# Optimization experiments

Measured on AMD Instinct MI355X. Metric: run time of the kernel, lower is better.

## Reference

```python
import jax, jax.numpy as jnp
import numpy as np

B = 4096      # batch of states
N = 32        # SVGD particles per state
D_ACT = 16    # action dim
D_OBS = 64    # obs dim
H = 256       # critic hidden width
STEPS = 3     # num_svgd_steps
LR = 0.1      # svgd_lr
LIMIT = 1.0   # act_limit


def q_mlp(obs, x, w1, b1, w2, b2, w3, b3):
    # SAC-style critic: q(obs, a) -> scalar per row. obs/x: [BN, *]
    h = jnp.concatenate([obs, x], axis=-1)
    h = jax.nn.relu(h @ w1 + b1)
    h = jax.nn.relu(h @ w2 + b2)
    return (h @ w3 + b3)[..., 0]  # [BN]


def rbf_kernel(X, Y):
    # X: [B, N, D] (differentiable), Y: [B, N, D] (detached copy of X)
    diff = X[:, :, None, :] - Y[:, None, :, :]          # [B, N, N, D]
    dist_sq = jnp.sum(diff * diff, axis=-1)             # [B, N, N]
    # median heuristic bandwidth per batch element
    med = jnp.median(dist_sq.reshape(dist_sq.shape[0], -1), axis=-1)
    h = med / np.log(N) + 1e-8
    gamma = jax.lax.stop_gradient(1.0 / (2.0 * h))      # [B]
    K = jnp.exp(-gamma[:, None, None] * dist_sq)        # [B, N, N]
    # dK/dX (grad wrt first argument)
    K_grad = -2.0 * gamma[:, None, None, None] * diff * K[..., None]  # [B,N,N,D]
    return K, diff, gamma, K_grad


def setup_inputs() -> dict:
    key = jax.random.key(0)
    ks = jax.random.split(key, 6)
    BN = B * N
    sc = lambda k, shp: jax.random.normal(k, shp, jnp.float32) * 0.05
    return {
        "obs": jax.random.normal(ks[0], (BN, D_OBS), jnp.float32),
        "a": jax.random.normal(ks[1], (BN, D_ACT), jnp.float32),
        "w1": sc(ks[2], (D_OBS + D_ACT, H)),
        "b1": jnp.zeros((H,), jnp.float32),
        "w2": sc(ks[3], (H, H)),
        "b2": jnp.zeros((H,), jnp.float32),
        "w3": sc(ks[4], (H, 1)),
        "b3": jnp.zeros((1,), jnp.float32),
    }


def reference(obs, a, w1, b1, w2, b2, w3, b3):
    # a0 arrives detached in the original (sampler(obs, a0.detach(), ...))
    a = jax.lax.stop_gradient(a)
    logp = jnp.zeros((B, N), jnp.float32)
    q_fn = lambda X: q_mlp(obs, X, w1, b1, w2, b2, w3, b3)
    q_vals = None
    for _ in range(STEPS):
        # log_prob = min(q1, q1) == q1; score = d(sum q)/dX via vjp
        q_vals, vjp_fn = jax.vjp(q_fn, a)                 # q_vals: [BN]
        score, = vjp_fn(jnp.ones_like(q_vals))            # [BN, D_ACT]
        X = a.reshape(B, N, D_ACT)
        S = score.reshape(B, N, D_ACT)
        K, diff, gamma, K_grad = rbf_kernel(X, jax.lax.stop_gradient(X))
        # phi = (K.detach() @ score - K_grad.sum(2)) / N
        drive = jnp.einsum('bij,bjd->bid', jax.lax.stop_gradient(K), S)
        phi = (drive - K_grad.sum(axis=2)) / N            # [B, N, D]
        # logp correction terms
        tmp1 = (K_grad * S[:, None, :, :]).sum(-1).mean(-1)                 # [B, N]
        tmp2 = -2.0 * gamma[:, None] * (((-K_grad) * diff).sum(-1)
                                        - D_ACT * K).mean(-1)               # [B, N]
        logp = logp - LR * (tmp1 + tmp2)
        # svgd_optim + clamp + detach
        a = a + LR * phi.reshape(B * N, D_ACT)
        a = jax.lax.stop_gradient(jnp.clip(a, -LIMIT, LIMIT))
    return a.reshape(B, N, D_ACT), logp, q_vals
```

## Files before the change

### kernel.cpp

```cpp
#include <hip/hip_runtime.h>
#include <hip/hip_bf16.h>
#include <math.h>

#define BNROWS (4096*32)
#define RB     64
#define LN32   3.4657359027997265f

typedef __attribute__((ext_vector_type(8))) short bf16x8;
typedef __attribute__((ext_vector_type(4))) float f32x4;

static __device__ __forceinline__ ushort f2bf(float x) {
    union { __hip_bfloat16 h; ushort u; } cv;
    cv.h = __float2bfloat16(x);
    return cv.u;
}

__global__ void prep_all(const float* __restrict__ obs,
                         ushort* __restrict__ obs_bf,
                         const float* __restrict__ w1,
                         const float* __restrict__ w2,
                         ushort* __restrict__ pB1, ushort* __restrict__ pB2,
                         ushort* __restrict__ pB3, ushort* __restrict__ pB4) {
    if (blockIdx.x < 8192) {
        size_t i = ((size_t)blockIdx.x * 256 + threadIdx.x) * 4;
        float4 v = *(const float4*)&obs[i];
        ushort4 o;
        o.x = f2bf(v.x); o.y = f2bf(v.y); o.z = f2bf(v.z); o.w = f2bf(v.w);
        *(ushort4*)&obs_bf[i] = o;
        return;
    }
    int g = (blockIdx.x - 8192) * 256 + threadIdx.x;
    ushort out[8];
    ushort* dst;
    if (g < 3072) {
        int lane = g & 63, gc = g >> 6;
        int t = gc / 3, c = gc % 3;
        int m = lane & 15, q = lane >> 4, n = t * 16 + m;
        #pragma unroll
        for (int j = 0; j < 8; ++j) {
            int k = c * 32 + q * 8 + j;
            out[j] = f2bf((k < 80) ? w1[k * 256 + n] : 0.f);
        }
        dst = &pB1[g * 8];
    } else if (g < 11264) {
        int gg = g - 3072;
        int lane = gg & 63, gc = gg >> 6;
        int t = gc >> 3, c = gc & 7;
        int m = lane & 15, q = lane >> 4, n = t * 16 + m;
        #pragma unroll
        for (int j = 0; j < 8; ++j)
            out[j] = f2bf(w2[(c * 32 + q * 8 + j) * 256 + n]);
        dst = &pB2[gg * 8];
    } else if (g < 19456) {
        int gg = g - 11264;
        int lane = gg & 63, gc = gg >> 6;
        int t = gc >> 3, c = gc & 7;
        int m = lane & 15, q = lane >> 4;
        #pragma unroll
        for (int j = 0; j < 8; ++j)
            out[j] = f2bf(w2[(t * 16 + m) * 256 + c * 32 + q * 8 + j]);
        dst = &pB3[gg * 8];
    } else if (g < 19968) {
        int gg = g - 19456;
        int lane = gg & 63, c = gg >> 6;
        int m = lane & 15, q = lane >> 4;
        #pragma unroll
        for (int j = 0; j < 8; ++j)
            out[j] = f2bf(w1[(64 + m) * 256 + c * 32 + q * 8 + j]);
        dst = &pB4[gg * 8];
    } else return;
    *(uint4*)dst = *(uint4*)out;
}

__global__ __launch_bounds__(512) void mlp_mfma(
    const ushort* __restrict__ obs_bf,
    const float* __restrict__ a_in,
    const float* __restrict__ b1,
    const float* __restrict__ b2,
    const float* __restrict__ w3,
    const float* __restrict__ b3,
    const ushort* __restrict__ pB1, const ushort* __restrict__ pB2,
    const ushort* __restrict__ pB3, const ushort* __restrict__ pB4,
    float* __restrict__ score,
    float* __restrict__ qout)
{
    __shared__ __align__(16) ushort B0[RB * 264];
    __shared__ __align__(16) ushort B1s[RB * 104];
    __shared__ float qpart[8][RB];
    __shared__ float bias1[256], bias2[256], w3s[256];

    const int tid  = threadIdx.x;
    const int row0 = blockIdx.x * RB;

    {
        int r = tid >> 3, ch = tid & 7;
        *(uint4*)&B1s[r * 104 + ch * 8] =
            *(const uint4*)&obs_bf[(size_t)(row0 + r) * 64 + ch * 8];
    }
    if (tid < 256) {
        int r = tid >> 2, d0 = (tid & 3) * 4;
        float4 av = *(const float4*)&a_in[(size_t)(row0 + r) * 16 + d0];
        ushort4 pv;
        pv.x = f2bf(av.x); pv.y = f2bf(av.y); pv.z = f2bf(av.z); pv.w = f2bf(av.w);
        *(ushort4*)&B1s[r * 104 + 64 + d0] = pv;
        ushort4 zv; zv.x = zv.y = zv.z = zv.w = 0;
        *(ushort4*)&B1s[r * 104 + 80 + d0] = zv;
        bias1[tid] = b1[tid]; bias2[tid] = b2[tid]; w3s[tid] = w3[tid];
    }
    __syncthreads();

    const int lane = tid & 63;
    const int w    = tid >> 6;
    const int m    = lane & 15;
    const int q    = lane >> 4;
    const int qk   = q * 8;

    f32x4 acc[4][2];
    unsigned relumask = 0u;

    #pragma unroll
    for (int tc = 0; tc < 2; ++tc)
        #pragma unroll
        for (int rt = 0; rt < 4; ++rt) acc[rt][tc] = (f32x4){0.f, 0.f, 0.f, 0.f};
    for (int c = 0; c < 3; ++c) {
        bf16x8 af[4];
        #pragma unroll
        for (int rt = 0; rt < 4; ++rt)
            af[rt] = *(const bf16x8*)&B1s[(rt * 16 + m) * 104 + c * 32 + qk];
        #pragma unroll
        for (int tc = 0; tc < 2; ++tc) {
            bf16x8 wfr = *(const bf16x8*)&pB1[(((w * 2 + tc) * 3 + c) * 64 + lane) * 8];
            #pragma unroll
            for (int rt = 0; rt < 4; ++rt)
                acc[rt][tc] = __builtin_amdgcn_mfma_f32_16x16x32_bf16(wfr, af[rt], acc[rt][tc], 0, 0, 0);
        }
    }
    #pragma unroll
    for (int tc = 0; tc < 2; ++tc) {
        const float4 bv = *(const float4*)&bias1[(w * 2 + tc) * 16 + q * 4];
        const float bva[4] = {bv.x, bv.y, bv.z, bv.w};
        #pragma unroll
        for (int rt = 0; rt < 4; ++rt) {
            ushort4 pk;
            float z0 = acc[rt][tc][0] + bva[0];
            float z1 = acc[rt][tc][1] + bva[1];
            float z2 = acc[rt][tc][2] + bva[2];
            float z3 = acc[rt][tc][3] + bva[3];
            if (z0 > 0.f) relumask |= 1u << (rt * 8 + tc * 4 + 0);
            if (z1 > 0.f) relumask |= 1u << (rt * 8 + tc * 4 + 1);
            if (z2 > 0.f) relumask |= 1u << (rt * 8 + tc * 4 + 2);
            if (z3 > 0.f) relumask |= 1u << (rt * 8 + tc * 4 + 3);
            pk.x = f2bf(fmaxf(z0, 0.f)); pk.y = f2bf(fmaxf(z1, 0.f));
            pk.z = f2bf(fmaxf(z2, 0.f)); pk.w = f2bf(fmaxf(z3, 0.f));
            *(ushort4*)&B0[(rt * 16 + m) * 264 + (w * 2 + tc) * 16 + q * 4] = pk;
        }
    }
    __syncthreads();

    #pragma unroll
    for (int tc = 0; tc < 2; ++tc)
        #pragma unroll
        for (int rt = 0; rt < 4; ++rt) acc[rt][tc] = (f32x4){0.f, 0.f, 0.f, 0.f};
    for (int c = 0; c < 8; ++c) {
        bf16x8 af[4];
        #pragma unroll
        for (int rt = 0; rt < 4; ++rt)
            af[rt] = *(const bf16x8*)&B0[(rt * 16 + m) * 264 + c * 32 + qk];
        #pragma unroll
        for (int tc = 0; tc < 2; ++tc) {
            bf16x8 wfr = *(const bf16x8*)&pB2[(((w * 2 + tc) * 8 + c) * 64 + lane) * 8];
            #pragma unroll
            for (int rt = 0; rt < 4; ++rt)
                acc[rt][tc] = __builtin_amdgcn_mfma_f32_16x16x32_bf16(wfr, af[rt], acc[rt][tc], 0, 0, 0);
        }
    }
    __syncthreads();
    {
        float qp[4] = {0.f, 0.f, 0.f, 0.f};
        #pragma unroll
        for (int tc = 0; tc < 2; ++tc) {
            const float4 bv = *(const float4*)&bias2[(w * 2 + tc) * 16 + q * 4];
            const float4 wv = *(const float4*)&w3s[(w * 2 + tc) * 16 + q * 4];
            const float bva[4] = {bv.x, bv.y, bv.z, bv.w};
            const float wva[4] = {wv.x, wv.y, wv.z, wv.w};
            #pragma unroll
            for (int rt = 0; rt < 4; ++rt) {
                ushort4 pk; float dz[4];
                #pragma unroll
                for (int i = 0; i < 4; ++i) {
                    float z = acc[rt][tc][i] + bva[i];
                    if (z > 0.f) { qp[rt] += z * wva[i]; dz[i] = wva[i]; }
                    else         { dz[i] = 0.f; }
                }
                pk.x = f2bf(dz[0]); pk.y = f2bf(dz[1]);
                pk.z = f2bf(dz[2]); pk.w = f2bf(dz[3]);
                *(ushort4*)&B0[(rt * 16 + m) * 264 + (w * 2 + tc) * 16 + q * 4] = pk;
            }
        }
        #pragma unroll
        for (int rt = 0; rt < 4; ++rt) {
            float v = qp[rt];
            v += __shfl_xor(v, 16); v += __shfl_xor(v, 32);
            if (q == 0) qpart[w][rt * 16 + m] = v;
        }
    }
    __syncthreads();

    if (tid < RB) {
        float qs = b3[0];
        #pragma unroll
        for (int ww = 0; ww < 8; ++ww) qs += qpart[ww][tid];
        qout[row0 + tid] = qs;
    }

    #pragma unroll
    for (int tc = 0; tc < 2; ++tc)
        #pragma unroll
        for (int rt = 0; rt < 4; ++rt) acc[rt][tc] = (f32x4){0.f, 0.f, 0.f, 0.f};
    for (int c = 0; c < 8; ++c) {
        bf16x8 af[4];
        #pragma unroll
        for (int rt = 0; rt < 4; ++rt)
            af[rt] = *(const bf16x8*)&B0[(rt * 16 + m) * 264 + c * 32 + qk];
        #pragma unroll
        for (int tc = 0; tc < 2; ++tc) {
            bf16x8 wfr = *(const bf16x8*)&pB3[(((w * 2 + tc) * 8 + c) * 64 + lane) * 8];
            #pragma unroll
            for (int rt = 0; rt < 4; ++rt)
                acc[rt][tc] = __builtin_amdgcn_mfma_f32_16x16x32_bf16(wfr, af[rt], acc[rt][tc], 0, 0, 0);
        }
    }
    __syncthreads();
    #pragma unroll
    for (int rt = 0; rt < 4; ++rt)
        #pragma unroll
        for (int tc = 0; tc < 2; ++tc) {
            ushort4 pk;
            pk.x = f2bf((relumask >> (rt * 8 + tc * 4 + 0)) & 1u ? acc[rt][tc][0] : 0.f);
            pk.y = f2bf((relumask >> (rt * 8 + tc * 4 + 1)) & 1u ? acc[rt][tc][1] : 0.f);
            pk.z = f2bf((relumask >> (rt * 8 + tc * 4 + 2)) & 1u ? acc[rt][tc][2] : 0.f);
            pk.w = f2bf((relumask >> (rt * 8 + tc * 4 + 3)) & 1u ? acc[rt][tc][3] : 0.f);
            *(ushort4*)&B0[(rt * 16 + m) * 264 + (w * 2 + tc) * 16 + q * 4] = pk;
        }
    __syncthreads();

    if (w < 4) {
        f32x4 acc2 = (f32x4){0.f, 0.f, 0.f, 0.f};
        for (int c = 0; c < 8; ++c) {
            bf16x8 af = *(const bf16x8*)&B0[(w * 16 + m) * 264 + c * 32 + qk];
            bf16x8 wfr = *(const bf16x8*)&pB4[(c * 64 + lane) * 8];
            acc2 = __builtin_amdgcn_mfma_f32_16x16x32_bf16(wfr, af, acc2, 0, 0, 0);
        }
        float4 o; o.x = acc2[0]; o.y = acc2[1]; o.z = acc2[2]; o.w = acc2[3];
        *(float4*)&score[(size_t)(row0 + w * 16 + m) * 16 + q * 4] = o;
    }
}

__global__ __launch_bounds__(256, 2) void svgd4(
    const float* __restrict__ a_in,
    const float* __restrict__ score,
    const float* __restrict__ logp_in,
    float* __restrict__ logp_out,
    float* __restrict__ a_out,
    int first)
{
    __shared__ __align__(16) float X4[4][32 * 20];
    __shared__ __align__(16) float S4[4][32 * 20];
    __shared__ __align__(16) float KM4[4][1024];

    const int tid    = threadIdx.x;
    const int wv     = tid >> 6;
    const int lane   = tid & 63;
    const int stateg = blockIdx.x * 4 + wv;
    const size_t base = (size_t)stateg * 512;

    float* X  = X4[wv];
    float* S  = S4[wv];
    float* KM = KM4[wv];
    int*   h  = (int*)KM4[wv];

    {
        int g0 = lane * 8;
        int r = g0 >> 4, d0 = g0 & 15;
        float4 va0 = *(const float4*)&a_in[base + g0];
        float4 va1 = *(const float4*)&a_in[base + g0 + 4];
        float4 vs0 = *(const float4*)&score[base + g0];
        float4 vs1 = *(const float4*)&score[base + g0 + 4];
        *(float4*)&X[r * 20 + d0]     = va0;
        *(float4*)&X[r * 20 + d0 + 4] = va1;
        *(float4*)&S[r * 20 + d0]     = vs0;
        *(float4*)&S[r * 20 + d0 + 4] = vs1;
    }
    __asm__ volatile("s_waitcnt lgkmcnt(0)" ::: "memory");

    const int half = lane >> 5;
    const int j    = lane & 31;

    float Xj[16], Sj[16];
    #pragma unroll
    for (int d0 = 0; d0 < 16; d0 += 4) {
        float4 xv = *(const float4*)&X[j * 20 + d0];
        float4 sv = *(const float4*)&S[j * 20 + d0];
        Xj[d0 + 0] = xv.x; Xj[d0 + 1] = xv.y; Xj[d0 + 2] = xv.z; Xj[d0 + 3] = xv.w;
        Sj[d0 + 0] = sv.x; Sj[d0 + 1] = sv.y; Sj[d0 + 2] = sv.z; Sj[d0 + 3] = sv.w;
    }

    unsigned v[16]; float p[16];
    #pragma unroll 4
    for (int t = 0; t < 16; ++t) {
        const float* Xi = &X[(half * 16 + t) * 20];
        float ss = 0.f, pp = 0.f;
        #pragma unroll
        for (int d0 = 0; d0 < 16; d0 += 4) {
            float4 xv = *(const float4*)&Xi[d0];
            float df0 = xv.x - Xj[d0 + 0];
            float df1 = xv.y - Xj[d0 + 1];
            float df2 = xv.z - Xj[d0 + 2];
            float df3 = xv.w - Xj[d0 + 3];
            ss = fmaf(df0, df0, ss); pp = fmaf(df0, Sj[d0 + 0], pp);
            ss = fmaf(df1, df1, ss); pp = fmaf(df1, Sj[d0 + 1], pp);
            ss = fmaf(df2, df2, ss); pp = fmaf(df2, Sj[d0 + 2], pp);
            ss = fmaf(df3, df3, ss); pp = fmaf(df3, Sj[d0 + 3], pp);
        }
        v[t] = __float_as_uint(ss);
        p[t] = pp;
    }

    unsigned prefix = 0;
    int rank = 511;
    #pragma unroll 1
    for (int pass = 0; pass < 4; ++pass) {
        const int sh = 24 - pass * 8;
        int4 z4; z4.x = z4.y = z4.z = z4.w = 0;
        *(int4*)&h[lane * 4] = z4;
        __asm__ volatile("s_waitcnt lgkmcnt(0)" ::: "memory");
        #pragma unroll
        for (int t = 0; t < 16; ++t) {
            bool ok = (pass == 0) || ((v[t] >> (sh + 8)) == prefix);
            if (ok) atomicAdd(&h[(v[t] >> sh) & 255], 1);
        }
        __asm__ volatile("s_waitcnt lgkmcnt(0)" ::: "memory");
        int4 c4 = *(const int4*)&h[lane * 4];
        int c[4] = {c4.x, c4.y, c4.z, c4.w};
        int ct = c[0] + c[1] + c[2] + c[3];
        int inc = ct;
        #pragma unroll
        for (int off = 1; off < 64; off <<= 1) {
            int tt = __shfl_up(inc, off, 64);
            if (lane >= off) inc += tt;
        }
        int run = inc - ct;
        int binf = -1, runf = 0;
        #pragma unroll
        for (int e = 0; e < 4; ++e) {
            if (binf < 0 && rank >= run && rank < run + c[e]) {
                binf = lane * 4 + e; runf = run;
            }
            run += c[e];
        }
        unsigned long long bm = __ballot(binf >= 0);
        int src = __ffsll(bm) - 1;
        int bin  = __shfl(binf, src);
        int excl = __shfl(runf, src);
        prefix = (prefix << 8) | (unsigned)bin;
        rank -= excl;
    }
    const float v1 = __uint_as_float(prefix);

    int cle = 0;
    unsigned mgt = 0xFFFFFFFFu;
    #pragma unroll
    for (int t = 0; t < 16; ++t) {
        if (v[t] <= prefix) cle++;
        else mgt = min(mgt, v[t]);
    }
    #pragma unroll
    for (int off = 1; off < 64; off <<= 1) {
        cle += __shfl_xor(cle, off);
        mgt = min(mgt, (unsigned)__shfl_xor((int)mgt, off));
    }
    const float v2  = (cle >= 513) ? v1 : __uint_as_float(mgt);
    const float med = 0.5f * (v1 + v2);
    const float gamma = 1.0f / (2.0f * (med / LN32 + 1e-8f));

    #pragma unroll 4
    for (int t = 0; t < 16; ++t) {
        int i = half * 16 + t;
        float kk = __expf(-gamma * __uint_as_float(v[t]));
        KM[i * 32 + (j ^ i)] = kk;
        float acc = fmaf(fmaf(2.f * gamma, __uint_as_float(v[t]), -16.f), kk,
                         kk * p[t]);
        #pragma unroll
        for (int off = 1; off < 32; off <<= 1)
            acc += __shfl_xor(acc, off);
        if (j == 0) {
            float tmp = -2.f * gamma * acc * (1.f / 32.f);
            float prev = first ? 0.f : logp_in[stateg * 32 + i];
            logp_out[stateg * 32 + i] = prev - 0.1f * tmp;
        }
    }
    __asm__ volatile("s_waitcnt lgkmcnt(0)" ::: "memory");

    {
        const int d  = lane & 15;
        const int i0 = lane >> 4;
        float s1[8], s2[8], xi[8];
        #pragma unroll
        for (int e = 0; e < 8; ++e) {
            s1[e] = 0.f; s2[e] = 0.f;
            xi[e] = X[(i0 + 4 * e) * 20 + d];
        }
        for (int jj = 0; jj < 32; ++jj) {
            float xjv = X[jj * 20 + d];
            float sjv = S[jj * 20 + d];
            #pragma unroll
            for (int e = 0; e < 8; ++e) {
                int i = i0 + 4 * e;
                float kk = KM[i * 32 + (jj ^ i)];
                s1[e] = fmaf(kk, sjv, s1[e]);
                s2[e] = fmaf(kk, xi[e] - xjv, s2[e]);
            }
        }
        #pragma unroll
        for (int e = 0; e < 8; ++e) {
            int i = i0 + 4 * e;
            float phi = (s1[e] + 2.f * gamma * s2[e]) * (1.f / 32.f);
            float av = xi[e] + 0.1f * phi;
            av = fminf(fmaxf(av, -1.f), 1.f);
            a_out[base + i * 16 + d] = av;
        }
    }
}

extern "C" void kernel_launch(void* const* d_in, const int* in_sizes, int n_in,
                              void* d_out, int out_size, void* d_ws, size_t ws_size,
                              hipStream_t stream) {
    const float* obs = (const float*)d_in[0];
    const float* a0  = (const float*)d_in[1];
    const float* w1  = (const float*)d_in[2];
    const float* b1  = (const float*)d_in[3];
    const float* w2  = (const float*)d_in[4];
    const float* b2  = (const float*)d_in[5];
    const float* w3  = (const float*)d_in[6];
    const float* b3  = (const float*)d_in[7];

    float* out_a    = (float*)d_out;
    float* out_logp = out_a + (size_t)BNROWS * 16;
    float* out_q    = out_logp + BNROWS;

    char* p = (char*)d_ws;
    ushort* pB1 = (ushort*)p; p += 24576 * 2;
    ushort* pB2 = (ushort*)p; p += 65536 * 2;
    ushort* pB3 = (ushort*)p; p += 65536 * 2;
    ushort* pB4 = (ushort*)p; p += 4096 * 2;
    ushort* obs_bf = (ushort*)p; p += (size_t)BNROWS * 64 * 2;
    float* abuf0 = (float*)p; p += (size_t)BNROWS * 16 * 4;
    float* abuf1 = (float*)p; p += (size_t)BNROWS * 16 * 4;
    float* scr   = (float*)p; p += (size_t)BNROWS * 16 * 4;
    float* logp  = (float*)p; p += (size_t)BNROWS * 4;
    float* qtmp  = (float*)p;

    prep_all<<<8270, 256, 0, stream>>>(obs, obs_bf, w1, w2, pB1, pB2, pB3, pB4);

    const int MB = BNROWS / RB;
    const int SB = 4096 / 4;

    mlp_mfma<<<MB, 512, 0, stream>>>(obs_bf, a0, b1, b2, w3, b3,
                                     pB1, pB2, pB3, pB4, scr, qtmp);
    svgd4<<<SB, 256, 0, stream>>>(a0, scr, nullptr, logp, abuf0, 1);
    mlp_mfma<<<MB, 512, 0, stream>>>(obs_bf, abuf0, b1, b2, w3, b3,
                                     pB1, pB2, pB3, pB4, scr, qtmp);
    svgd4<<<SB, 256, 0, stream>>>(abuf0, scr, logp, logp, abuf1, 0);
    mlp_mfma<<<MB, 512, 0, stream>>>(obs_bf, abuf1, b1, b2, w3, b3,
                                     pB1, pB2, pB3, pB4, scr, out_q);
    svgd4<<<SB, 256, 0, stream>>>(abuf1, scr, logp, out_logp, out_a, 0);
}
```

Before: 340.8 us.

## Split each SVGD state across two waves instead of one

The SVGD kernel now assigns two wavefronts (128 threads) per state instead of one, halving per-thread pair work and register arrays. The radix-select median uses per-wave histograms merged through shared memory with block barriers, and the count/min reduction is combined across waves. This doubles thread-level parallelism for the SVGD phase at the cost of extra __syncthreads and cross-wave shared-memory traffic.

```diff
diff --git a/kernel.cpp b/kernel.cpp
--- a/kernel.cpp
+++ b/kernel.cpp
@@ -256,7 +256,7 @@
     }
 }
 
-__global__ __launch_bounds__(256, 2) void svgd4(
+__global__ __launch_bounds__(256) void svgd5(
     const float* __restrict__ a_in,
     const float* __restrict__ score,
     const float* __restrict__ logp_in,
@@ -264,97 +264,91 @@
     float* __restrict__ a_out,
     int first)
 {
-    __shared__ __align__(16) float X4[4][32 * 20];
-    __shared__ __align__(16) float S4[4][32 * 20];
-    __shared__ __align__(16) float KM4[4][1024];
-
-    const int tid    = threadIdx.x;
-    const int wv     = tid >> 6;
-    const int lane   = tid & 63;
-    const int stateg = blockIdx.x * 4 + wv;
+    __shared__ __align__(16) float X2[2][32 * 20];
+    __shared__ __align__(16) float S2[2][32 * 20];
+    __shared__ __align__(16) float KM2[2][1024];
+    __shared__ int      cellC[2][2];
+    __shared__ unsigned cellM[2][2];
+
+    const int tid = threadIdx.x;
+    const int st  = tid >> 7;
+    const int th  = tid & 127;
+    const int h   = (tid >> 6) & 1;
+    const int l   = tid & 63;
+    const int j   = l & 31;
+    const int ibase = h * 16 + (l >> 5) * 8;
+
+    const int stateg  = blockIdx.x * 2 + st;
     const size_t base = (size_t)stateg * 512;
 
-    float* X  = X4[wv];
-    float* S  = S4[wv];
-    float* KM = KM4[wv];
-    int*   h  = (int*)KM4[wv];
+    float* X  = X2[st];
+    float* S  = S2[st];
+    float* KM = KM2[st];
+    int*   hist = (int*)KM2[st];
 
     {
-        int g0 = lane * 8;
-        int r = g0 >> 4, d0 = g0 & 15;
-        float4 va0 = *(const float4*)&a_in[base + g0];
-        float4 va1 = *(const float4*)&a_in[base + g0 + 4];
-        float4 vs0 = *(const float4*)&score[base + g0];
-        float4 vs1 = *(const float4*)&score[base + g0 + 4];
-        *(float4*)&X[r * 20 + d0]     = va0;
-        *(float4*)&X[r * 20 + d0 + 4] = va1;
-        *(float4*)&S[r * 20 + d0]     = vs0;
-        *(float4*)&S[r * 20 + d0 + 4] = vs1;
-    }
-    __asm__ volatile("s_waitcnt lgkmcnt(0)" ::: "memory");
-
-    const int half = lane >> 5;
-    const int j    = lane & 31;
-
-    float Xj[16], Sj[16];
-    #pragma unroll
+        float4 va = *(const float4*)&a_in[base + th * 4];
+        float4 vs = *(const float4*)&score[base + th * 4];
+        int r = th >> 2, d0 = (th & 3) * 4;
+        *(float4*)&X[r * 20 + d0] = va;
+        *(float4*)&S[r * 20 + d0] = vs;
+    }
+    __syncthreads();
+
+    float ss[8], pp[8];
+    #pragma unroll
+    for (int t = 0; t < 8; ++t) { ss[t] = 0.f; pp[t] = 0.f; }
+    #pragma unroll 1
     for (int d0 = 0; d0 < 16; d0 += 4) {
-        float4 xv = *(const float4*)&X[j * 20 + d0];
-        float4 sv = *(const float4*)&S[j * 20 + d0];
-        Xj[d0 + 0] = xv.x; Xj[d0 + 1] = xv.y; Xj[d0 + 2] = xv.z; Xj[d0 + 3] = xv.w;
-        Sj[d0 + 0] = sv.x; Sj[d0 + 1] = sv.y; Sj[d0 + 2] = sv.z; Sj[d0 + 3] = sv.w;
-    }
-
-    unsigned v[16]; float p[16];
-    #pragma unroll 4
-    for (int t = 0; t < 16; ++t) {
-        const float* Xi = &X[(half * 16 + t) * 20];
-        float ss = 0.f, pp = 0.f;
-        #pragma unroll
-        for (int d0 = 0; d0 < 16; d0 += 4) {
-            float4 xv = *(const float4*)&Xi[d0];
-            float df0 = xv.x - Xj[d0 + 0];
-            float df1 = xv.y - Xj[d0 + 1];
-            float df2 = xv.z - Xj[d0 + 2];
-            float df3 = xv.w - Xj[d0 + 3];
-            ss = fmaf(df0, df0, ss); pp = fmaf(df0, Sj[d0 + 0], pp);
-            ss = fmaf(df1, df1, ss); pp = fmaf(df1, Sj[d0 + 1], pp);
-            ss = fmaf(df2, df2, ss); pp = fmaf(df2, Sj[d0 + 2], pp);
-            ss = fmaf(df3, df3, ss); pp = fmaf(df3, Sj[d0 + 3], pp);
-        }
-        v[t] = __float_as_uint(ss);
-        p[t] = pp;
-    }
+        float4 xj = *(const float4*)&X[j * 20 + d0];
+        float4 sj = *(const float4*)&S[j * 20 + d0];
+        #pragma unroll
+        for (int t = 0; t < 8; ++t) {
+            float4 xi = *(const float4*)&X[(ibase + t) * 20 + d0];
+            float df0 = xi.x - xj.x, df1 = xi.y - xj.y;
+            float df2 = xi.z - xj.z, df3 = xi.w - xj.w;
+            ss[t] = fmaf(df0, df0, ss[t]); pp[t] = fmaf(df0, sj.x, pp[t]);
+            ss[t] = fmaf(df1, df1, ss[t]); pp[t] = fmaf(df1, sj.y, pp[t]);
+            ss[t] = fmaf(df2, df2, ss[t]); pp[t] = fmaf(df2, sj.z, pp[t]);
+            ss[t] = fmaf(df3, df3, ss[t]); pp[t] = fmaf(df3, sj.w, pp[t]);
+        }
+    }
+    unsigned v[8];
+    #pragma unroll
+    for (int t = 0; t < 8; ++t) v[t] = __float_as_uint(ss[t]);
 
     unsigned prefix = 0;
     int rank = 511;
     #pragma unroll 1
     for (int pass = 0; pass < 4; ++pass) {
         const int sh = 24 - pass * 8;
+        int* hreg  = hist + (pass & 1) * 512;
+        int* hmine = hreg + h * 256;
         int4 z4; z4.x = z4.y = z4.z = z4.w = 0;
-        *(int4*)&h[lane * 4] = z4;
+        *(int4*)&hmine[l * 4] = z4;
         __asm__ volatile("s_waitcnt lgkmcnt(0)" ::: "memory");
         #pragma unroll
-        for (int t = 0; t < 16; ++t) {
+        for (int t = 0; t < 8; ++t) {
             bool ok = (pass == 0) || ((v[t] >> (sh + 8)) == prefix);
-            if (ok) atomicAdd(&h[(v[t] >> sh) & 255], 1);
-        }
-        __asm__ volatile("s_waitcnt lgkmcnt(0)" ::: "memory");
-        int4 c4 = *(const int4*)&h[lane * 4];
-        int c[4] = {c4.x, c4.y, c4.z, c4.w};
+            if (ok) atomicAdd(&hmine[(v[t] >> sh) & 255], 1);
+        }
+        __syncthreads();
+        int4 c0 = *(const int4*)&hreg[l * 4];
+        int4 c1 = *(const int4*)&hreg[256 + l * 4];
+        int c[4] = {c0.x + c1.x, c0.y + c1.y, c0.z + c1.z, c0.w + c1.w};
         int ct = c[0] + c[1] + c[2] + c[3];
         int inc = ct;
         #pragma unroll
         for (int off = 1; off < 64; off <<= 1) {
             int tt = __shfl_up(inc, off, 64);
-            if (lane >= off) inc += tt;
+            if (l >= off) inc += tt;
         }
         int run = inc - ct;
         int binf = -1, runf = 0;
         #pragma unroll
         for (int e = 0; e < 4; ++e) {
             if (binf < 0 && rank >= run && rank < run + c[e]) {
-                binf = lane * 4 + e; runf = run;
+                binf = l * 4 + e; runf = run;
             }
             run += c[e];
         }
@@ -367,29 +361,35 @@
     }
     const float v1 = __uint_as_float(prefix);
 
-    int cle = 0;
-    unsigned mgt = 0xFFFFFFFFu;
-    #pragma unroll
-    for (int t = 0; t < 16; ++t) {
-        if (v[t] <= prefix) cle++;
-        else mgt = min(mgt, v[t]);
-    }
-    #pragma unroll
-    for (int off = 1; off < 64; off <<= 1) {
-        cle += __shfl_xor(cle, off);
-        mgt = min(mgt, (unsigned)__shfl_xor((int)mgt, off));
-    }
-    const float v2  = (cle >= 513) ? v1 : __uint_as_float(mgt);
-    const float med = 0.5f * (v1 + v2);
+    {
+        int cle = 0;
+        unsigned mgt = 0xFFFFFFFFu;
+        #pragma unroll
+        for (int t = 0; t < 8; ++t) {
+            if (v[t] <= prefix) cle++;
+            else mgt = min(mgt, v[t]);
+        }
+        #pragma unroll
+        for (int off = 1; off < 64; off <<= 1) {
+            cle += __shfl_xor(cle, off);
+            mgt = min(mgt, (unsigned)__shfl_xor((int)mgt, off));
+        }
+        if (l == 0) { cellC[st][h] = cle; cellM[st][h] = mgt; }
+    }
+    __syncthreads();
+    const int C      = cellC[st][0] + cellC[st][1];
+    const unsigned M = min(cellM[st][0], cellM[st][1]);
+    const float v2   = (C >= 513) ? v1 : __uint_as_float(M);
+    const float med  = 0.5f * (v1 + v2);
     const float gamma = 1.0f / (2.0f * (med / LN32 + 1e-8f));
 
     #pragma unroll 4
-    for (int t = 0; t < 16; ++t) {
-        int i = half * 16 + t;
+    for (int t = 0; t < 8; ++t) {
+        int i = ibase + t;
         float kk = __expf(-gamma * __uint_as_float(v[t]));
         KM[i * 32 + (j ^ i)] = kk;
         float acc = fmaf(fmaf(2.f * gamma, __uint_as_float(v[t]), -16.f), kk,
-                         kk * p[t]);
+                         kk * pp[t]);
         #pragma unroll
         for (int off = 1; off < 32; off <<= 1)
             acc += __shfl_xor(acc, off);
@@ -399,31 +399,31 @@
             logp_out[stateg * 32 + i] = prev - 0.1f * tmp;
         }
     }
-    __asm__ volatile("s_waitcnt lgkmcnt(0)" ::: "memory");
+    __syncthreads();
 
     {
-        const int d  = lane & 15;
-        const int i0 = lane >> 4;
-        float s1[8], s2[8], xi[8];
-        #pragma unroll
-        for (int e = 0; e < 8; ++e) {
+        const int d  = th & 15;
+        const int i0 = th >> 4;
+        float s1[4], s2[4], xi[4];
+        #pragma unroll
+        for (int e = 0; e < 4; ++e) {
             s1[e] = 0.f; s2[e] = 0.f;
-            xi[e] = X[(i0 + 4 * e) * 20 + d];
+            xi[e] = X[(i0 + 8 * e) * 20 + d];
         }
         for (int jj = 0; jj < 32; ++jj) {
             float xjv = X[jj * 20 + d];
             float sjv = S[jj * 20 + d];
             #pragma unroll
-            for (int e = 0; e < 8; ++e) {
-                int i = i0 + 4 * e;
+            for (int e = 0; e < 4; ++e) {
+                int i = i0 + 8 * e;
                 float kk = KM[i * 32 + (jj ^ i)];
                 s1[e] = fmaf(kk, sjv, s1[e]);
                 s2[e] = fmaf(kk, xi[e] - xjv, s2[e]);
             }
         }
         #pragma unroll
-        for (int e = 0; e < 8; ++e) {
-            int i = i0 + 4 * e;
+        for (int e = 0; e < 4; ++e) {
+            int i = i0 + 8 * e;
             float phi = (s1[e] + 2.f * gamma * s2[e]) * (1.f / 32.f);
             float av = xi[e] + 0.1f * phi;
             av = fminf(fmaxf(av, -1.f), 1.f);
@@ -463,15 +463,15 @@
     prep_all<<<8270, 256, 0, stream>>>(obs, obs_bf, w1, w2, pB1, pB2, pB3, pB4);
 
     const int MB = BNROWS / RB;
-    const int SB = 4096 / 4;
+    const int SB = 4096 / 2;
 
     mlp_mfma<<<MB, 512, 0, stream>>>(obs_bf, a0, b1, b2, w3, b3,
                                      pB1, pB2, pB3, pB4, scr, qtmp);
-    svgd4<<<SB, 256, 0, stream>>>(a0, scr, nullptr, logp, abuf0, 1);
+    svgd5<<<SB, 256, 0, stream>>>(a0, scr, nullptr, logp, abuf0, 1);
     mlp_mfma<<<MB, 512, 0, stream>>>(obs_bf, abuf0, b1, b2, w3, b3,
                                      pB1, pB2, pB3, pB4, scr, qtmp);
-    svgd4<<<SB, 256, 0, stream>>>(abuf0, scr, logp, logp, abuf1, 0);
+    svgd5<<<SB, 256, 0, stream>>>(abuf0, scr, logp, logp, abuf1, 0);
     mlp_mfma<<<MB, 512, 0, stream>>>(obs_bf, abuf1, b1, b2, w3, b3,
                                      pB1, pB2, pB3, pB4, scr, out_q);
-    svgd4<<<SB, 256, 0, stream>>>(abuf1, scr, logp, out_logp, out_a, 0);
+    svgd5<<<SB, 256, 0, stream>>>(abuf1, scr, logp, out_logp, out_a, 0);
 }
```

New measurement: 351.1 us. 1.03x slower.
